# Kernel optimization log

Measured on AMD Instinct MI355X. Metric: run time of the kernel, lower is better.

## Reference

```python
import jax, jax.numpy as jnp
import numpy as np

B, H, W, C = 8, 64, 64, 512
DQK = C // 8  # query/key channel dim from Conv2D(filters//8, 1)


def setup_inputs() -> dict:
    key = jax.random.key(0)
    ks = jax.random.split(key, 8)
    s_in = 1.0 / np.sqrt(C)
    x = jax.random.normal(ks[0], (B, H, W, C), dtype=jnp.float32)
    Wq = jax.random.normal(ks[1], (C, DQK), dtype=jnp.float32) * s_in
    bq = jnp.zeros((DQK,), dtype=jnp.float32)
    Wk = jax.random.normal(ks[2], (C, DQK), dtype=jnp.float32) * s_in
    bk = jnp.zeros((DQK,), dtype=jnp.float32)
    Wv = jax.random.normal(ks[3], (C, C), dtype=jnp.float32) * s_in
    bv = jnp.zeros((C,), dtype=jnp.float32)
    # gamma initialized to zeros in the original, but use a nonzero value so
    # the attention branch actually contributes to the output/gradients.
    gamma = jnp.ones((1,), dtype=jnp.float32) * 0.5
    return {"x": x, "Wq": Wq, "bq": bq, "Wk": Wk, "bk": bk,
            "Wv": Wv, "bv": bv, "gamma": gamma}


def reference(x, Wq, bq, Wk, bk, Wv, bv, gamma):
    b, h, w, c = x.shape
    n = h * w  # spatial_size
    xf = x.reshape(b, n, c)
    # 1x1 convs == per-pixel channel matmuls
    q = xf @ Wq + bq            # [B, N, C//8]
    k = xf @ Wk + bk            # [B, N, C//8]
    v = xf @ Wv + bv            # [B, N, C]
    # Dot(axes=-1): attn[b,i,j] = sum_d q[b,i,d] * k[b,j,d]
    attn = jnp.einsum('bid,bjd->bij', q, k)
    attn = jax.nn.softmax(attn, axis=-1)
    # Dot(axes=-2): out[b,j,c] = sum_i attn[b,i,j] * v[b,i,c]  (note transpose)
    out = jnp.einsum('bij,bic->bjc', attn, v)
    out = out.reshape(b, h, w, c)
    return gamma * out + x
```

## Files before the change

kernel.cpp:

```cpp
#include <hip/hip_runtime.h>
#include <hip/hip_bf16.h>
#include <cstdio>

typedef unsigned short u16;
typedef __attribute__((ext_vector_type(4))) float f32x4;
typedef __attribute__((ext_vector_type(8))) short s16x8;

__device__ __forceinline__ u16 bf16b(float f) {
  union { float f; unsigned u; } c; c.f = f;
  unsigned u = c.u;
  return (u16)((u + 0x7FFFu + ((u >> 16) & 1u)) >> 16);
}

__device__ __forceinline__ void load16(const void* g, void* l) {
  __builtin_amdgcn_global_load_lds(
      (const __attribute__((address_space(1))) void*)g,
      (__attribute__((address_space(3))) void*)l, 16, 0, 0);
}


__global__ __launch_bounds__(256) void cvt_x_k(const float* __restrict__ x,
                                               u16* __restrict__ xb) {
  long i = ((long)blockIdx.x * 256 + threadIdx.x) * 4;
  float4 f = *(const float4*)&x[i];
  unsigned lo = (unsigned)bf16b(f.x) | ((unsigned)bf16b(f.y) << 16);
  unsigned hi = (unsigned)bf16b(f.z) | ((unsigned)bf16b(f.w) << 16);
  uint2 v; v.x = lo; v.y = hi;
  *(uint2*)&xb[i] = v;
}

__global__ __launch_bounds__(256) void cvt_w_k(const float* __restrict__ Wq,
                                               const float* __restrict__ Wk,
                                               const float* __restrict__ Wv,
                                               u16* __restrict__ Wcat) {
  int idx = blockIdx.x * 256 + threadIdx.x;
  int nn = idx >> 9, k = idx & 511;
  float v;
  if (nn < 64)       v = Wq[k * 64 + nn];
  else if (nn < 128) v = Wk[k * 64 + (nn - 64)];
  else               v = Wv[k * 512 + (nn - 128)];
  Wcat[idx] = bf16b(v);
}

__global__ __launch_bounds__(256) void transV_k(const u16* __restrict__ Vr,
                                                u16* __restrict__ Vt) {
  __shared__ u16 t[64][66];
  const int b = blockIdx.z;
  const long i0 = (long)blockIdx.x * 64, c0 = (long)blockIdx.y * 64;
  const u16* src = Vr + (long)b * 4096 * 512;
  u16* dst = Vt + (long)b * 512 * 4096;
  const int tid = threadIdx.x;
#pragma unroll
  for (int p = 0; p < 16; ++p) {
    int idx = p * 256 + tid;
    int r = idx >> 6, c = idx & 63;
    t[r][c] = src[(i0 + r) * 512 + c0 + c];
  }
  __syncthreads();
#pragma unroll
  for (int p = 0; p < 16; ++p) {
    int idx = p * 256 + tid;
    int r = idx >> 6, c = idx & 63;
    dst[(c0 + r) * 4096 + i0 + c] = t[c][r];
  }
}

template <int BM, int BN, int EPI>
__global__ __launch_bounds__(256, 2) void gemmT(
    const u16* __restrict__ A, const u16* __restrict__ B, int K, int lda,
    int ldb, long sA, long sB, void* p0, void* p1, void* p2, void* p3,
    void* p4, void* p5, long s0, long s1, long s2) {
  constexpr int FM = BM / 32, FN = BN / 32;
  __shared__ __align__(16) u16 At[BM * 64];
  __shared__ __align__(16) u16 Bt[BN * 64];
  const int tid = threadIdx.x;
  const int lane = tid & 63, w = tid >> 6;
  const int wr = w >> 1, wc = w & 1;
  const int l15 = lane & 15, lhi = lane >> 4;
  const long m0 = (long)blockIdx.x * BM;
  const long n0 = (long)blockIdx.y * BN;
  const int z = blockIdx.z;
  A += (long)z * sA;
  B += (long)z * sB;
  char* b0 = (char*)p0 + (long)z * s0;
  char* b1 = (char*)p1 + (long)z * s1;
  char* b2 = (char*)p2 + (long)z * s2;

  f32x4 acc[FM][FN] = {};

  for (int k0 = 0; k0 < K; k0 += 64) {
#pragma unroll
    for (int it = 0; it < (BM + BN) * 8 / 256; ++it) {
      int q = it * 256 + tid;
      if (q < BM * 8) {
        int row = q >> 3, c8 = q & 7;
        load16(A + (m0 + row) * lda + k0 + c8 * 8, &At[q * 8]);
      } else {
        int q2 = q - BM * 8;
        int row = q2 >> 3, c8 = q2 & 7;
        load16(B + (n0 + row) * ldb + k0 + c8 * 8, &Bt[q2 * 8]);
      }
    }
    __syncthreads();
#pragma unroll
    for (int kk = 0; kk < 64; kk += 32) {
      s16x8 af[FM], bf[FN];
#pragma unroll
      for (int i = 0; i < FM; ++i)
        af[i] = *(const s16x8*)&At[(wr * (BM / 2) + i * 16 + l15) * 64 + kk + lhi * 8];
#pragma unroll
      for (int j = 0; j < FN; ++j)
        bf[j] = *(const s16x8*)&Bt[(wc * (BN / 2) + j * 16 + l15) * 64 + kk + lhi * 8];
#pragma unroll
      for (int i = 0; i < FM; ++i)
#pragma unroll
        for (int j = 0; j < FN; ++j)
          acc[i][j] = __builtin_amdgcn_mfma_f32_16x16x32_bf16(af[i], bf[j],
                                                              acc[i][j], 0, 0, 0);
    }
    __syncthreads();
  }

#pragma unroll
  for (int i = 0; i < FM; ++i) {
#pragma unroll
    for (int j = 0; j < FN; ++j) {
      long mm = m0 + wr * (BM / 2) + i * 16 + lhi * 4;
      long nn = n0 + wc * (BN / 2) + j * 16 + l15;
#pragma unroll
      for (int r = 0; r < 4; ++r) {
        long m = mm + r;
        float v = acc[i][j][r];
        if constexpr (EPI == 0) {
          if (nn < 64) {
            v += ((const float*)p3)[nn];
            ((u16*)b0)[m * 64 + nn] = bf16b(v);
          } else if (nn < 128) {
            v += ((const float*)p4)[nn - 64];
            ((u16*)b1)[m * 64 + nn - 64] = bf16b(v);
          } else {
            v += ((const float*)p5)[nn - 128];
            ((u16*)b2)[m * 512 + nn - 128] = bf16b(v);
          }
        }
      }
    }
  }
}

__global__ __launch_bounds__(256, 2) void stats_k(const u16* __restrict__ Qb,
                                                  const u16* __restrict__ Kb,
                                                  float* __restrict__ m_part,
                                                  float* __restrict__ l_part) {
  const int b = blockIdx.z, jc = blockIdx.y;
  const long i0 = (long)blockIdx.x * 128;
  const u16* Q = Qb + (long)b * 4096 * 64;
  const u16* Kp = Kb + (long)b * 4096 * 64;
  __shared__ __align__(16) u16 Qt[128 * 64];
  __shared__ __align__(16) u16 Kt[128 * 64];
  const int tid = threadIdx.x, lane = tid & 63, w = tid >> 6;
  const int l15 = lane & 15, lhi = lane >> 4;

#pragma unroll
  for (int it = 0; it < 4; ++it) {
    int q = it * 256 + tid;
    int row = q >> 3, c8 = q & 7;
    load16(Q + (i0 + row) * 64 + c8 * 8, &Qt[q * 8]);
  }

  float mrun[2][4], lrun[2][4];
#pragma unroll
  for (int i = 0; i < 2; ++i)
#pragma unroll
    for (int r = 0; r < 4; ++r) { mrun[i][r] = -1e30f; lrun[i][r] = 0.f; }

  for (int jt = 0; jt < 8; ++jt) {
    long j0 = (long)jc * 1024 + jt * 128;
#pragma unroll
    for (int it = 0; it < 4; ++it) {
      int q = it * 256 + tid;
      int row = q >> 3, c8 = q & 7;
      load16(Kp + (j0 + row) * 64 + c8 * 8, &Kt[q * 8]);
    }
    __syncthreads();
    f32x4 acc[2][8] = {};
#pragma unroll
    for (int kk = 0; kk < 64; kk += 32) {
      s16x8 af[2], bf[8];
#pragma unroll
      for (int i = 0; i < 2; ++i)
        af[i] = *(const s16x8*)&Qt[(w * 32 + i * 16 + l15) * 64 + kk + lhi * 8];
#pragma unroll
      for (int j = 0; j < 8; ++j)
        bf[j] = *(const s16x8*)&Kt[(j * 16 + l15) * 64 + kk + lhi * 8];
#pragma unroll
      for (int i = 0; i < 2; ++i)
#pragma unroll
        for (int j = 0; j < 8; ++j)
          acc[i][j] = __builtin_amdgcn_mfma_f32_16x16x32_bf16(af[i], bf[j],
                                                              acc[i][j], 0, 0, 0);
    }
#pragma unroll
    for (int i = 0; i < 2; ++i)
#pragma unroll
      for (int r = 0; r < 4; ++r) {
        float tm = acc[i][0][r];
#pragma unroll
        for (int j = 1; j < 8; ++j) tm = fmaxf(tm, acc[i][j][r]);
        float mo = mrun[i][r];
        float mn = fmaxf(mo, tm);
        float s = 0.f;
#pragma unroll
        for (int j = 0; j < 8; ++j) s += __expf(acc[i][j][r] - mn);
        lrun[i][r] = lrun[i][r] * __expf(mo - mn) + s;
        mrun[i][r] = mn;
      }
    __syncthreads();
  }

#pragma unroll
  for (int i = 0; i < 2; ++i)
#pragma unroll
    for (int r = 0; r < 4; ++r) {
      float m = mrun[i][r], l = lrun[i][r];
#pragma unroll
      for (int d = 1; d < 16; d <<= 1) {
        float mo = __shfl_xor(m, d);
        float lo = __shfl_xor(l, d);
        float mn = fmaxf(m, mo);
        l = l * __expf(m - mn) + lo * __expf(mo - mn);
        m = mn;
      }
      if (l15 == 0) {
        long ig = i0 + w * 32 + i * 16 + lhi * 4 + r;
        long idx = ((long)(b * 4 + jc)) * 4096 + ig;
        m_part[idx] = m;
        l_part[idx] = l;
      }
    }
}

__global__ __launch_bounds__(256) void merge_k(const float* __restrict__ m_part,
                                               const float* __restrict__ l_part,
                                               float* __restrict__ mfin,
                                               float* __restrict__ linv) {
  int idx = blockIdx.x * 256 + threadIdx.x;
  int b = idx >> 12, i = idx & 4095;
  float m = -1e30f, l = 0.f;
#pragma unroll
  for (int jc = 0; jc < 4; ++jc) {
    long o = ((long)(b * 4 + jc)) * 4096 + i;
    float mp = m_part[o], lp = l_part[o];
    float mn = fmaxf(m, mp);
    l = l * __expf(m - mn) + lp * __expf(mp - mn);
    m = mn;
  }
  mfin[idx] = m;
  linv[idx] = 1.0f / l;
}

__global__ __launch_bounds__(256, 2) void fusedPV(
    const u16* __restrict__ Qb, const u16* __restrict__ Kb,
    const u16* __restrict__ Vt, const float* __restrict__ mfin,
    const float* __restrict__ lnv, const float* __restrict__ x,
    const float* __restrict__ gamma, float* __restrict__ out) {
  __shared__ __align__(16) u16 Kt[128 * 64];
  __shared__ __align__(16) u16 Qc[64 * 64];
  __shared__ __align__(16) u16 Vc[256 * 64];
  __shared__ __align__(16) u16 Pl[128 * 64];
  __shared__ __align__(16) float Ml[64];
  __shared__ __align__(16) float Ll[64];
  const int tid = threadIdx.x, lane = tid & 63, w = tid >> 6;
  const int l15 = lane & 15, lhi = lane >> 4;
  const int wi = w & 1, wj = w >> 1, wc = w & 1;
  const int b = blockIdx.z;
  const long j0 = (long)blockIdx.x * 128;
  const long c0 = (long)blockIdx.y * 256;
  const u16* Qg = Qb + (long)b * 4096 * 64;
  const u16* Kg = Kb + (long)b * 4096 * 64;
  const u16* Vg = Vt + (long)b * 512 * 4096;
  const float* mg = mfin + (long)b * 4096;
  const float* lg = lnv + (long)b * 4096;

#pragma unroll
  for (int p = 0; p < 4; ++p) {
    int s = p * 256 + tid;
    int r = s >> 3, col = s & 7, cg = col ^ (r & 7);
    load16(Kg + (j0 + r) * 64 + cg * 8, (char*)Kt + r * 128 + col * 16);
  }

  f32x4 acc2[4][8] = {};
  const float gma = gamma[0];

  for (int t = 0; t < 64; ++t) {
    const int i_base = t * 64;
#pragma unroll
    for (int p = 0; p < 2; ++p) {
      int s = p * 256 + tid;
      int r = s >> 3, col = s & 7, cg = col ^ (r & 7);
      load16(Qg + (long)(i_base + r) * 64 + cg * 8,
             (char*)Qc + r * 128 + col * 16);
    }
#pragma unroll
    for (int p = 0; p < 8; ++p) {
      int s = p * 256 + tid;
      int r = s >> 3, col = s & 7, cg = col ^ (r & 7);
      load16(Vg + (c0 + r) * 4096 + i_base + cg * 8,
             (char*)Vc + r * 128 + col * 16);
    }
    if (tid < 64) {
      Ml[tid] = mg[i_base + tid];
      Ll[tid] = lg[i_base + tid];
    }
    __syncthreads();

    f32x4 acc1[2][4] = {};
#pragma unroll
    for (int kk = 0; kk < 64; kk += 32) {
      s16x8 af[2], bk4[4];
#pragma unroll
      for (int fi = 0; fi < 2; ++fi) {
        int r = wi * 32 + fi * 16 + l15;
        af[fi] = *(const s16x8*)((const char*)Qc + r * 128 +
                                 (((kk + lhi * 8) * 2) ^ ((r & 7) << 4)));
      }
#pragma unroll
      for (int fj = 0; fj < 4; ++fj) {
        int r = wj * 64 + fj * 16 + l15;
        bk4[fj] = *(const s16x8*)((const char*)Kt + r * 128 +
                                  (((kk + lhi * 8) * 2) ^ ((r & 7) << 4)));
      }
#pragma unroll
      for (int fi = 0; fi < 2; ++fi)
#pragma unroll
        for (int fj = 0; fj < 4; ++fj)
          acc1[fi][fj] = __builtin_amdgcn_mfma_f32_16x16x32_bf16(
              af[fi], bk4[fj], acc1[fi][fj], 0, 0, 0);
    }

#pragma unroll
    for (int fi = 0; fi < 2; ++fi) {
      int i0l = wi * 32 + fi * 16 + lhi * 4;
      f32x4 mv = *(const f32x4*)&Ml[i0l];
      f32x4 lv = *(const f32x4*)&Ll[i0l];
#pragma unroll
      for (int fj = 0; fj < 4; ++fj) {
        int j = wj * 64 + fj * 16 + l15;
        float p0 = __expf(acc1[fi][fj][0] - mv[0]) * lv[0];
        float p1 = __expf(acc1[fi][fj][1] - mv[1]) * lv[1];
        float p2 = __expf(acc1[fi][fj][2] - mv[2]) * lv[2];
        float p3 = __expf(acc1[fi][fj][3] - mv[3]) * lv[3];
        unsigned u01 = (unsigned)bf16b(p0) | ((unsigned)bf16b(p1) << 16);
        unsigned u23 = (unsigned)bf16b(p2) | ((unsigned)bf16b(p3) << 16);
        char* base = (char*)Pl + j * 128;
        int byt = (i0l * 2) ^ ((j & 7) << 4);
        *(unsigned*)(base + byt) = u01;
        *(unsigned*)(base + byt + 4) = u23;
      }
    }
    __syncthreads();

#pragma unroll
    for (int kk = 0; kk < 64; kk += 32) {
      s16x8 pa[4];
#pragma unroll
      for (int fm = 0; fm < 4; ++fm) {
        int r = wj * 64 + fm * 16 + l15;
        pa[fm] = *(const s16x8*)((const char*)Pl + r * 128 +
                                 (((kk + lhi * 8) * 2) ^ ((r & 7) << 4)));
      }
#pragma unroll
      for (int fn = 0; fn < 8; ++fn) {
        int r = wc * 128 + fn * 16 + l15;
        s16x8 vb = *(const s16x8*)((const char*)Vc + r * 128 +
                                   (((kk + lhi * 8) * 2) ^ ((r & 7) << 4)));
#pragma unroll
        for (int fm = 0; fm < 4; ++fm)
          acc2[fm][fn] = __builtin_amdgcn_mfma_f32_16x16x32_bf16(
              pa[fm], vb, acc2[fm][fn], 0, 0, 0);
      }
    }
    __syncthreads();
  }

#pragma unroll
  for (int fm = 0; fm < 4; ++fm) {
#pragma unroll
    for (int fn = 0; fn < 8; ++fn) {
      long j = j0 + wj * 64 + fm * 16 + lhi * 4;
      long c = c0 + wc * 128 + fn * 16 + l15;
#pragma unroll
      for (int r = 0; r < 4; ++r) {
        long o = ((long)b * 4096 + j + r) * 512 + c;
        out[o] = gma * acc2[fm][fn][r] + x[o];
      }
    }
  }
}


extern "C" void kernel_launch(void* const* d_in, const int* in_sizes, int n_in,
                              void* d_out, int out_size, void* d_ws,
                              size_t ws_size, hipStream_t stream) {
  const float* x = (const float*)d_in[0];
  const float* Wq = (const float*)d_in[1];
  const float* bq = (const float*)d_in[2];
  const float* Wk = (const float*)d_in[3];
  const float* bk = (const float*)d_in[4];
  const float* Wv = (const float*)d_in[5];
  const float* bv = (const float*)d_in[6];
  const float* gamma = (const float*)d_in[7];
  float* out = (float*)d_out;

  char* ws = (char*)d_ws;
  size_t off = 0;
  auto alloc = [&](size_t bytes) {
    char* p = ws + off;
    off += (bytes + 255) & ~(size_t)255;
    return p;
  };
  u16* xb = (u16*)alloc((size_t)32768 * 512 * 2);
  u16* Wcat = (u16*)alloc((size_t)640 * 512 * 2);
  u16* Qb = (u16*)alloc((size_t)8 * 4096 * 64 * 2);
  u16* Kb = (u16*)alloc((size_t)8 * 4096 * 64 * 2);
  u16* Vr = (u16*)alloc((size_t)8 * 4096 * 512 * 2);
  u16* Vt = (u16*)alloc((size_t)8 * 512 * 4096 * 2);
  float* m_part = (float*)alloc((size_t)8 * 4 * 4096 * 4);
  float* l_part = (float*)alloc((size_t)8 * 4 * 4096 * 4);
  float* mfin = (float*)alloc((size_t)8 * 4096 * 4);
  float* lnv = (float*)alloc((size_t)8 * 4096 * 4);
  if (off > ws_size) {
    fprintf(stderr, "kernel_launch: ws too small: need %zu have %zu\n", off,
            ws_size);
    return;
  }

  cvt_w_k<<<1280, 256, 0, stream>>>(Wq, Wk, Wv, Wcat);
  cvt_x_k<<<16384, 256, 0, stream>>>(x, xb);
  gemmT<128, 128, 0><<<dim3(256, 5, 1), 256, 0, stream>>>(
      xb, Wcat, 512, 512, 512, 0, 0, Qb, Kb, Vr, (void*)bq, (void*)bk,
      (void*)bv, 0, 0, 0);
  transV_k<<<dim3(64, 8, 8), 256, 0, stream>>>(Vr, Vt);
  stats_k<<<dim3(32, 4, 8), 256, 0, stream>>>(Qb, Kb, m_part, l_part);
  merge_k<<<128, 256, 0, stream>>>(m_part, l_part, mfin, lnv);
  fusedPV<<<dim3(32, 2, 8), 256, 0, stream>>>(Qb, Kb, Vt, mfin, lnv, x,
                                              gamma, out);
}
```

Baseline: 325.6 us.

## Fuse V transpose into projection GEMM and double-buffer fusedPV with 512 threads

The projection GEMM epilogue now writes V directly in transposed layout, which removes the separate transpose kernel and the intermediate V buffer. fusedPV moves to 512-thread blocks covering 256 j-rows, and double-buffers the Q and V chunk loads so the next tile is fetched while the current one is computed. It reads the softmax max and inverse sum straight from global memory instead of staging them in LDS, and uses raw s_waitcnt/s_barrier asm in place of __syncthreads. Risks include the larger LDS footprint (about 136KB) limiting occupancy, fewer blocks (256) across the CUs, and uncoalesced 8-byte strided stores of Vt in the GEMM epilogue.

```diff
diff --git a/kernel.cpp b/kernel.cpp
--- a/kernel.cpp
+++ b/kernel.cpp
@@ -17,6 +17,9 @@
       (const __attribute__((address_space(1))) void*)g,
       (__attribute__((address_space(3))) void*)l, 16, 0, 0);
 }
+
+#define BARV() asm volatile("s_waitcnt vmcnt(0) lgkmcnt(0)\n\ts_barrier" ::: "memory")
+#define BAR() asm volatile("s_waitcnt lgkmcnt(0)\n\ts_barrier" ::: "memory")
 
 
 __global__ __launch_bounds__(256) void cvt_x_k(const float* __restrict__ x,
@@ -42,35 +45,12 @@
   Wcat[idx] = bf16b(v);
 }
 
-__global__ __launch_bounds__(256) void transV_k(const u16* __restrict__ Vr,
-                                                u16* __restrict__ Vt) {
-  __shared__ u16 t[64][66];
-  const int b = blockIdx.z;
-  const long i0 = (long)blockIdx.x * 64, c0 = (long)blockIdx.y * 64;
-  const u16* src = Vr + (long)b * 4096 * 512;
-  u16* dst = Vt + (long)b * 512 * 4096;
-  const int tid = threadIdx.x;
-#pragma unroll
-  for (int p = 0; p < 16; ++p) {
-    int idx = p * 256 + tid;
-    int r = idx >> 6, c = idx & 63;
-    t[r][c] = src[(i0 + r) * 512 + c0 + c];
-  }
-  __syncthreads();
-#pragma unroll
-  for (int p = 0; p < 16; ++p) {
-    int idx = p * 256 + tid;
-    int r = idx >> 6, c = idx & 63;
-    dst[(c0 + r) * 4096 + i0 + c] = t[c][r];
-  }
-}
-
-template <int BM, int BN, int EPI>
-__global__ __launch_bounds__(256, 2) void gemmT(
-    const u16* __restrict__ A, const u16* __restrict__ B, int K, int lda,
-    int ldb, long sA, long sB, void* p0, void* p1, void* p2, void* p3,
-    void* p4, void* p5, long s0, long s1, long s2) {
-  constexpr int FM = BM / 32, FN = BN / 32;
+__global__ __launch_bounds__(256, 2) void projGemm(
+    const u16* __restrict__ A, const u16* __restrict__ B,
+    u16* __restrict__ Qb, u16* __restrict__ Kb, u16* __restrict__ Vt,
+    const float* __restrict__ bq, const float* __restrict__ bk,
+    const float* __restrict__ bv) {
+  constexpr int BM = 128, BN = 128, FM = 4, FN = 4;
   __shared__ __align__(16) u16 At[BM * 64];
   __shared__ __align__(16) u16 Bt[BN * 64];
   const int tid = threadIdx.x;
@@ -79,26 +59,20 @@
   const int l15 = lane & 15, lhi = lane >> 4;
   const long m0 = (long)blockIdx.x * BM;
   const long n0 = (long)blockIdx.y * BN;
-  const int z = blockIdx.z;
-  A += (long)z * sA;
-  B += (long)z * sB;
-  char* b0 = (char*)p0 + (long)z * s0;
-  char* b1 = (char*)p1 + (long)z * s1;
-  char* b2 = (char*)p2 + (long)z * s2;
 
   f32x4 acc[FM][FN] = {};
 
-  for (int k0 = 0; k0 < K; k0 += 64) {
-#pragma unroll
-    for (int it = 0; it < (BM + BN) * 8 / 256; ++it) {
+  for (int k0 = 0; k0 < 512; k0 += 64) {
+#pragma unroll
+    for (int it = 0; it < 8; ++it) {
       int q = it * 256 + tid;
       if (q < BM * 8) {
         int row = q >> 3, c8 = q & 7;
-        load16(A + (m0 + row) * lda + k0 + c8 * 8, &At[q * 8]);
+        load16(A + (m0 + row) * 512 + k0 + c8 * 8, &At[q * 8]);
       } else {
         int q2 = q - BM * 8;
         int row = q2 >> 3, c8 = q2 & 7;
-        load16(B + (n0 + row) * ldb + k0 + c8 * 8, &Bt[q2 * 8]);
+        load16(B + (n0 + row) * 512 + k0 + c8 * 8, &Bt[q2 * 8]);
       }
     }
     __syncthreads();
@@ -107,10 +81,10 @@
       s16x8 af[FM], bf[FN];
 #pragma unroll
       for (int i = 0; i < FM; ++i)
-        af[i] = *(const s16x8*)&At[(wr * (BM / 2) + i * 16 + l15) * 64 + kk + lhi * 8];
+        af[i] = *(const s16x8*)&At[(wr * 64 + i * 16 + l15) * 64 + kk + lhi * 8];
 #pragma unroll
       for (int j = 0; j < FN; ++j)
-        bf[j] = *(const s16x8*)&Bt[(wc * (BN / 2) + j * 16 + l15) * 64 + kk + lhi * 8];
+        bf[j] = *(const s16x8*)&Bt[(wc * 64 + j * 16 + l15) * 64 + kk + lhi * 8];
 #pragma unroll
       for (int i = 0; i < FM; ++i)
 #pragma unroll
@@ -125,24 +99,27 @@
   for (int i = 0; i < FM; ++i) {
 #pragma unroll
     for (int j = 0; j < FN; ++j) {
-      long mm = m0 + wr * (BM / 2) + i * 16 + lhi * 4;
-      long nn = n0 + wc * (BN / 2) + j * 16 + l15;
-#pragma unroll
-      for (int r = 0; r < 4; ++r) {
-        long m = mm + r;
-        float v = acc[i][j][r];
-        if constexpr (EPI == 0) {
-          if (nn < 64) {
-            v += ((const float*)p3)[nn];
-            ((u16*)b0)[m * 64 + nn] = bf16b(v);
-          } else if (nn < 128) {
-            v += ((const float*)p4)[nn - 64];
-            ((u16*)b1)[m * 64 + nn - 64] = bf16b(v);
-          } else {
-            v += ((const float*)p5)[nn - 128];
-            ((u16*)b2)[m * 512 + nn - 128] = bf16b(v);
-          }
-        }
+      long mm = m0 + wr * 64 + i * 16 + lhi * 4;
+      long nn = n0 + wc * 64 + j * 16 + l15;
+      if (nn < 64) {
+        float bb = bq[nn];
+#pragma unroll
+        for (int r = 0; r < 4; ++r)
+          Qb[(mm + r) * 64 + nn] = bf16b(acc[i][j][r] + bb);
+      } else if (nn < 128) {
+        float bb = bk[nn - 64];
+#pragma unroll
+        for (int r = 0; r < 4; ++r)
+          Kb[(mm + r) * 64 + nn - 64] = bf16b(acc[i][j][r] + bb);
+      } else {
+        long c = nn - 128;
+        float bb = bv[c];
+        unsigned u01 = (unsigned)bf16b(acc[i][j][0] + bb) |
+                       ((unsigned)bf16b(acc[i][j][1] + bb) << 16);
+        unsigned u23 = (unsigned)bf16b(acc[i][j][2] + bb) |
+                       ((unsigned)bf16b(acc[i][j][3] + bb) << 16);
+        uint2 u; u.x = u01; u.y = u23;
+        *(uint2*)&Vt[(mm >> 12) * 512 * 4096 + c * 4096 + (mm & 4095)] = u;
       }
     }
   }
@@ -259,22 +236,20 @@
   linv[idx] = 1.0f / l;
 }
 
-__global__ __launch_bounds__(256, 2) void fusedPV(
+__global__ __launch_bounds__(512, 2) void fusedPV(
     const u16* __restrict__ Qb, const u16* __restrict__ Kb,
     const u16* __restrict__ Vt, const float* __restrict__ mfin,
     const float* __restrict__ lnv, const float* __restrict__ x,
     const float* __restrict__ gamma, float* __restrict__ out) {
-  __shared__ __align__(16) u16 Kt[128 * 64];
-  __shared__ __align__(16) u16 Qc[64 * 64];
-  __shared__ __align__(16) u16 Vc[256 * 64];
-  __shared__ __align__(16) u16 Pl[128 * 64];
-  __shared__ __align__(16) float Ml[64];
-  __shared__ __align__(16) float Ll[64];
+  __shared__ __align__(16) u16 Kt[256 * 64];
+  __shared__ __align__(16) u16 Qc[2][64 * 64];
+  __shared__ __align__(16) u16 Vc[2][256 * 64];
+  __shared__ __align__(16) u16 Pl[256 * 64];
   const int tid = threadIdx.x, lane = tid & 63, w = tid >> 6;
   const int l15 = lane & 15, lhi = lane >> 4;
   const int wi = w & 1, wj = w >> 1, wc = w & 1;
   const int b = blockIdx.z;
-  const long j0 = (long)blockIdx.x * 128;
+  const long j0 = (long)blockIdx.x * 256;
   const long c0 = (long)blockIdx.y * 256;
   const u16* Qg = Qb + (long)b * 4096 * 64;
   const u16* Kg = Kb + (long)b * 4096 * 64;
@@ -284,35 +259,42 @@
 
 #pragma unroll
   for (int p = 0; p < 4; ++p) {
-    int s = p * 256 + tid;
+    int s = p * 512 + tid;
     int r = s >> 3, col = s & 7, cg = col ^ (r & 7);
     load16(Kg + (j0 + r) * 64 + cg * 8, (char*)Kt + r * 128 + col * 16);
   }
+  {
+    int r = tid >> 3, col = tid & 7, cg = col ^ (r & 7);
+    load16(Qg + (long)r * 64 + cg * 8, (char*)&Qc[0][0] + r * 128 + col * 16);
+#pragma unroll
+    for (int p = 0; p < 4; ++p) {
+      int s = p * 512 + tid;
+      int r2 = s >> 3, c2 = s & 7, cg2 = c2 ^ (r2 & 7);
+      load16(Vg + (c0 + r2) * 4096 + cg2 * 8,
+             (char*)&Vc[0][0] + r2 * 128 + c2 * 16);
+    }
+  }
 
   f32x4 acc2[4][8] = {};
   const float gma = gamma[0];
+  int cur = 0;
 
   for (int t = 0; t < 64; ++t) {
     const int i_base = t * 64;
-#pragma unroll
-    for (int p = 0; p < 2; ++p) {
-      int s = p * 256 + tid;
-      int r = s >> 3, col = s & 7, cg = col ^ (r & 7);
-      load16(Qg + (long)(i_base + r) * 64 + cg * 8,
-             (char*)Qc + r * 128 + col * 16);
-    }
-#pragma unroll
-    for (int p = 0; p < 8; ++p) {
-      int s = p * 256 + tid;
-      int r = s >> 3, col = s & 7, cg = col ^ (r & 7);
-      load16(Vg + (c0 + r) * 4096 + i_base + cg * 8,
-             (char*)Vc + r * 128 + col * 16);
-    }
-    if (tid < 64) {
-      Ml[tid] = mg[i_base + tid];
-      Ll[tid] = lg[i_base + tid];
-    }
-    __syncthreads();
+    BARV();
+    if (t < 63) {
+      const long ib2 = (long)(t + 1) * 64;
+      int r = tid >> 3, col = tid & 7, cg = col ^ (r & 7);
+      load16(Qg + (ib2 + r) * 64 + cg * 8,
+             (char*)&Qc[cur ^ 1][0] + r * 128 + col * 16);
+#pragma unroll
+      for (int p = 0; p < 4; ++p) {
+        int s = p * 512 + tid;
+        int r2 = s >> 3, c2 = s & 7, cg2 = c2 ^ (r2 & 7);
+        load16(Vg + (c0 + r2) * 4096 + ib2 + cg2 * 8,
+               (char*)&Vc[cur ^ 1][0] + r2 * 128 + c2 * 16);
+      }
+    }
 
     f32x4 acc1[2][4] = {};
 #pragma unroll
@@ -321,7 +303,7 @@
 #pragma unroll
       for (int fi = 0; fi < 2; ++fi) {
         int r = wi * 32 + fi * 16 + l15;
-        af[fi] = *(const s16x8*)((const char*)Qc + r * 128 +
+        af[fi] = *(const s16x8*)((const char*)&Qc[cur][0] + r * 128 +
                                  (((kk + lhi * 8) * 2) ^ ((r & 7) << 4)));
       }
 #pragma unroll
@@ -341,8 +323,8 @@
 #pragma unroll
     for (int fi = 0; fi < 2; ++fi) {
       int i0l = wi * 32 + fi * 16 + lhi * 4;
-      f32x4 mv = *(const f32x4*)&Ml[i0l];
-      f32x4 lv = *(const f32x4*)&Ll[i0l];
+      f32x4 mv = *(const f32x4*)&mg[i_base + i0l];
+      f32x4 lv = *(const f32x4*)&lg[i_base + i0l];
 #pragma unroll
       for (int fj = 0; fj < 4; ++fj) {
         int j = wj * 64 + fj * 16 + l15;
@@ -358,7 +340,7 @@
         *(unsigned*)(base + byt + 4) = u23;
       }
     }
-    __syncthreads();
+    BAR();
 
 #pragma unroll
     for (int kk = 0; kk < 64; kk += 32) {
@@ -372,7 +354,7 @@
 #pragma unroll
       for (int fn = 0; fn < 8; ++fn) {
         int r = wc * 128 + fn * 16 + l15;
-        s16x8 vb = *(const s16x8*)((const char*)Vc + r * 128 +
+        s16x8 vb = *(const s16x8*)((const char*)&Vc[cur][0] + r * 128 +
                                    (((kk + lhi * 8) * 2) ^ ((r & 7) << 4)));
 #pragma unroll
         for (int fm = 0; fm < 4; ++fm)
@@ -380,7 +362,7 @@
               pa[fm], vb, acc2[fm][fn], 0, 0, 0);
       }
     }
-    __syncthreads();
+    cur ^= 1;
   }
 
 #pragma unroll
@@ -423,7 +405,6 @@
   u16* Wcat = (u16*)alloc((size_t)640 * 512 * 2);
   u16* Qb = (u16*)alloc((size_t)8 * 4096 * 64 * 2);
   u16* Kb = (u16*)alloc((size_t)8 * 4096 * 64 * 2);
-  u16* Vr = (u16*)alloc((size_t)8 * 4096 * 512 * 2);
   u16* Vt = (u16*)alloc((size_t)8 * 512 * 4096 * 2);
   float* m_part = (float*)alloc((size_t)8 * 4 * 4096 * 4);
   float* l_part = (float*)alloc((size_t)8 * 4 * 4096 * 4);
@@ -437,12 +418,10 @@
 
   cvt_w_k<<<1280, 256, 0, stream>>>(Wq, Wk, Wv, Wcat);
   cvt_x_k<<<16384, 256, 0, stream>>>(x, xb);
-  gemmT<128, 128, 0><<<dim3(256, 5, 1), 256, 0, stream>>>(
-      xb, Wcat, 512, 512, 512, 0, 0, Qb, Kb, Vr, (void*)bq, (void*)bk,
-      (void*)bv, 0, 0, 0);
-  transV_k<<<dim3(64, 8, 8), 256, 0, stream>>>(Vr, Vt);
+  projGemm<<<dim3(256, 5, 1), 256, 0, stream>>>(xb, Wcat, Qb, Kb, Vt, bq, bk,
+                                                bv);
   stats_k<<<dim3(32, 4, 8), 256, 0, stream>>>(Qb, Kb, m_part, l_part);
   merge_k<<<128, 256, 0, stream>>>(m_part, l_part, mfin, lnv);
-  fusedPV<<<dim3(32, 2, 8), 256, 0, stream>>>(Qb, Kb, Vt, mfin, lnv, x,
+  fusedPV<<<dim3(16, 2, 8), 512, 0, stream>>>(Qb, Kb, Vt, mfin, lnv, x,
                                               gamma, out);
 }
```

Result: faster. 314.4 us (-3.4%).
